# Optimization experiments

Measured on AMD Instinct MI355X. Metric: run time of the kernel, lower is better.

The kernel has to match this reference:

```python
import jax, jax.numpy as jnp
import numpy as np

N = 100000      # nodes
E = 640000      # total edges across all relations
D_IN = 128
D_OUT = 128
R = 8           # num_rel
B = 4           # num_bases


def setup_inputs() -> dict:
    key = jax.random.key(0)
    ks = jax.random.split(key, 7)
    return {
        "X": jax.random.normal(ks[0], (N, D_IN), dtype=jnp.float32),
        "edge_src": jax.random.randint(ks[1], (E,), 0, N, dtype=jnp.int32),
        "edge_dst": jax.random.randint(ks[2], (E,), 0, N, dtype=jnp.int32),
        "edge_rel": jax.random.randint(ks[3], (E,), 0, R, dtype=jnp.int32),
        "edge_val": jax.random.uniform(ks[4], (E,), dtype=jnp.float32),
        "w_bases": jax.random.normal(ks[5], (B, D_IN, D_OUT), dtype=jnp.float32) * 0.05,
        "w_rel": jax.random.normal(ks[6], (R, B), dtype=jnp.float32) * 0.5,
    }


def reference(X, edge_src, edge_dst, edge_rel, edge_val, w_bases, w_rel):
    # Per-relation SpMM: support_r = A_r @ X, where A_r rows are destinations.
    # Fuse all relations into one gather + one segmented scatter-add.
    msg = X[edge_src] * edge_val[:, None]                      # [E, D_IN]
    seg = edge_rel.astype(jnp.int32) * N + edge_dst            # combined (rel, dst) id
    supports = jax.ops.segment_sum(msg, seg, num_segments=R * N)
    supports = supports.reshape(R, N, D_IN)                    # == concat of per-rel supports
    # Basis-decomposed relation weights: w[r] = sum_b w_rel[r,b] * w_bases[b]
    w = jnp.einsum("rb,bio->rio", w_rel, w_bases)              # [R, D_IN, D_OUT]
    # cat(supports, dim=1) @ w.view(R*D_IN, D_OUT) == sum_r supports_r @ w_r
    out = jnp.einsum("rni,rio->no", supports, w)               # [N, D_OUT]
    return out
```

## Files before the change

### kernel.cpp

```cpp
#include <hip/hip_runtime.h>
#include <stdint.h>

#define D_IN 128
#define D_OUT 128
#define NREL 8
#define NBASE 4

typedef __attribute__((ext_vector_type(8))) short short8;
typedef __attribute__((ext_vector_type(4))) float floatx4;
typedef __attribute__((ext_vector_type(2))) float floatx2;

__device__ __forceinline__ unsigned short f2bf(float f) {
  unsigned int u = __float_as_uint(f);
  u += 0x7fffu + ((u >> 16) & 1u);
  return (unsigned short)(u >> 16);
}
__device__ __forceinline__ unsigned pack2bf(float lo, float hi) {
  return (unsigned)f2bf(lo) | ((unsigned)f2bf(hi) << 16);
}
__device__ __forceinline__ float bflo(unsigned int u) { return __uint_as_float(u << 16); }
__device__ __forceinline__ float bfhi(unsigned int u) { return __uint_as_float(u & 0xffff0000u); }

__global__ void k_prep(const float4* __restrict__ X, ushort4* __restrict__ Xb, int n4,
                       const float* __restrict__ w_bases, unsigned short* __restrict__ W2T,
                       const int* __restrict__ edst, int* __restrict__ counts, int E) {
  int i = blockIdx.x * blockDim.x + threadIdx.x;
  if (i < n4) {
    float4 v = X[i];
    ushort4 o;
    o.x = f2bf(v.x); o.y = f2bf(v.y); o.z = f2bf(v.z); o.w = f2bf(v.w);
    Xb[i] = o;
  }
  if (i < 128 * 512) {
    int o = i >> 9, c = i & 511;
    int k = c >> 2, b = c & 3;
    W2T[i] = f2bf(w_bases[(b * D_IN + k) * D_OUT + o]);
  }
  if (i < E) atomicAdd(&counts[edst[i]], 1);
}

__global__ void k_scan1(const int* __restrict__ counts, int* __restrict__ localsc,
                        int* __restrict__ bsum, int Nn) {
  __shared__ int s[256];
  int i = blockIdx.x * 256 + threadIdx.x;
  int v = (i < Nn) ? counts[i] : 0;
  s[threadIdx.x] = v;
  __syncthreads();
  for (int off = 1; off < 256; off <<= 1) {
    int t = 0;
    if (threadIdx.x >= off) t = s[threadIdx.x - off];
    __syncthreads();
    s[threadIdx.x] += t;
    __syncthreads();
  }
  if (i < Nn) localsc[i] = s[threadIdx.x] - v;
  if (threadIdx.x == 255) bsum[blockIdx.x] = s[255];
}

__global__ void k_scan23(const int* __restrict__ localsc, const int* __restrict__ bsum,
                         int* __restrict__ offsets, int* __restrict__ cursor, int Nn, int E) {
  __shared__ int red[256];
  int acc = 0;
  for (int j = threadIdx.x; j < blockIdx.x; j += 256) acc += bsum[j];
  red[threadIdx.x] = acc;
  __syncthreads();
  for (int off = 128; off > 0; off >>= 1) {
    if (threadIdx.x < off) red[threadIdx.x] += red[threadIdx.x + off];
    __syncthreads();
  }
  int pref = red[0];
  int i = blockIdx.x * 256 + threadIdx.x;
  if (i < Nn) {
    int v = localsc[i] + pref;
    offsets[i] = v;
    cursor[i] = v;
  }
  if (i == 0) offsets[Nn] = E;
}

__global__ void k_bucket(const int* __restrict__ src, const int* __restrict__ dst,
                         const int* __restrict__ rel, const float* __restrict__ val,
                         const float* __restrict__ w_rel, int* __restrict__ cursor,
                         unsigned* __restrict__ srcs, float4* __restrict__ coef, int E) {
  int i = blockIdx.x * blockDim.x + threadIdx.x;
  if (i < 64) srcs[E + i] = 0u;
  if (i >= E) return;
  int d = dst[i];
  int pos = atomicAdd(&cursor[d], 1);
  float v = val[i];
  const float4 w = *(const float4*)(w_rel + rel[i] * 4);
  srcs[pos] = (unsigned)src[i];
  coef[pos] = make_float4(v * w.x, v * w.y, v * w.z, v * w.w);
}

__global__ __launch_bounds__(256, 4)
void k_agg_gemm(const unsigned* __restrict__ esrcs, const float4* __restrict__ ecoef,
                const int* __restrict__ offsets, const unsigned* __restrict__ Xb2,
                const unsigned short* __restrict__ W2T, float* __restrict__ out, int Nn) {
  __shared__ __align__(16) unsigned short aggS[32][520];

  const int wave = threadIdx.x >> 6, lane = threadIdx.x & 63;
  const int d0 = blockIdx.x * 32 + wave * 8;
  const floatx2 zf2 = {0.f, 0.f};
  const uint64_t xbase = (uint64_t)Xb2;
  const unsigned loff = (unsigned)lane * 4u;

  int oidx = d0 + (lane < 8 ? lane : 8);
  if (oidx > Nn) oidx = Nn;
  const int offv = offsets[oidx];
  const int s0 = __builtin_amdgcn_readlane(offv, 0);
  const int e8 = __builtin_amdgcn_readlane(offv, 8);

  floatx2 a0 = zf2, a1 = zf2, a2 = zf2, a3 = zf2;
  int row = 0;
  int bnd = __builtin_amdgcn_readlane(offv, 1);

#define FLUSH()                                                      \
  do {                                                               \
    uint4 o_;                                                        \
    o_.x = pack2bf(a0.x, a1.x);                                      \
    o_.y = pack2bf(a2.x, a3.x);                                      \
    o_.z = pack2bf(a0.y, a1.y);                                      \
    o_.w = pack2bf(a2.y, a3.y);                                      \
    *(uint4*)&aggS[wave * 8 + row][lane * 8] = o_;                   \
    a0 = zf2; a1 = zf2; a2 = zf2; a3 = zf2;                          \
    ++row;                                                           \
    bnd = (row < 8) ? __builtin_amdgcn_readlane(offv, row + 1)       \
                    : 0x7fffffff;                                    \
  } while (0)

#define SSRC(S, BASE)                                                \
  do {                                                               \
    int b_ = (BASE);                                                 \
    s##S##0 = esrcs[b_];     s##S##1 = esrcs[b_ + 1];                \
    s##S##2 = esrcs[b_ + 2]; s##S##3 = esrcs[b_ + 3];                \
  } while (0)

#define GLOAD(Y, SRCID)                                              \
  do {                                                               \
    uint64_t ga_ = xbase + ((uint64_t)(SRCID) << 8);                 \
    asm volatile("global_load_dword %0, %1, %2"                      \
                 : "=v"(Y) : "v"(loff), "s"(ga_));                   \
  } while (0)

#define GATH(S)                                                      \
  do {                                                               \
    GLOAD(y##S##0, s##S##0); GLOAD(y##S##1, s##S##1);                \
    GLOAD(y##S##2, s##S##2); GLOAD(y##S##3, s##S##3);                \
  } while (0)

#define SCOEF(S, BASE)                                               \
  do {                                                               \
    int b_ = (BASE);                                                 \
    c##S##0 = ecoef[b_];     c##S##1 = ecoef[b_ + 1];                \
    c##S##2 = ecoef[b_ + 2]; c##S##3 = ecoef[b_ + 3];                \
  } while (0)

#define WAITG()                                                      \
  do {                                                               \
    asm volatile("s_waitcnt vmcnt(12)" ::: "memory");                \
    __builtin_amdgcn_sched_barrier(0);                               \
  } while (0)

#define ACCT1(EI, C, Y)                                              \
  do {                                                               \
    if ((EI) < e8) {                                                 \
      while ((EI) == bnd) FLUSH();                                   \
      floatx2 x_;                                                    \
      x_.x = bflo(Y);                                                \
      x_.y = bfhi(Y);                                                \
      a0 += (C).x * x_;                                              \
      a1 += (C).y * x_;                                              \
      a2 += (C).z * x_;                                              \
      a3 += (C).w * x_;                                              \
    }                                                                \
  } while (0)

#define ACCT4(S, EI0)                                                \
  do {                                                               \
    ACCT1((EI0), c##S##0, y##S##0);                                  \
    ACCT1((EI0) + 1, c##S##1, y##S##1);                              \
    ACCT1((EI0) + 2, c##S##2, y##S##2);                              \
    ACCT1((EI0) + 3, c##S##3, y##S##3);                              \
  } while (0)

  if (s0 < e8) {
    unsigned s00, s01, s02, s03, s10, s11, s12, s13, s20, s21, s22, s23;
    unsigned s30, s31, s32, s33, s40, s41, s42, s43, s50, s51, s52, s53;
    unsigned y00, y01, y02, y03, y10, y11, y12, y13, y20, y21, y22, y23;
    unsigned y30, y31, y32, y33, y40, y41, y42, y43, y50, y51, y52, y53;
    float4 c00, c01, c02, c03, c10, c11, c12, c13, c20, c21, c22, c23;
    float4 c30, c31, c32, c33, c40, c41, c42, c43, c50, c51, c52, c53;
    SSRC(0, s0); SSRC(1, s0 + 4); SSRC(2, s0 + 8); SSRC(3, s0 + 12);
    GATH(0); GATH(1); GATH(2);
    SCOEF(0, s0);
    int gi = s0;
    while (gi < e8) {
      GATH(3); SSRC(4, gi + 16); SCOEF(1, gi + 4);  WAITG(); ACCT4(0, gi);
      GATH(4); SSRC(5, gi + 20); SCOEF(2, gi + 8);  WAITG(); ACCT4(1, gi + 4);
      GATH(5); SSRC(0, gi + 24); SCOEF(3, gi + 12); WAITG(); ACCT4(2, gi + 8);
      GATH(0); SSRC(1, gi + 28); SCOEF(4, gi + 16); WAITG(); ACCT4(3, gi + 12);
      GATH(1); SSRC(2, gi + 32); SCOEF(5, gi + 20); WAITG(); ACCT4(4, gi + 16);
      GATH(2); SSRC(3, gi + 36); SCOEF(0, gi + 24); WAITG(); ACCT4(5, gi + 20);
      gi += 24;
    }
    __builtin_amdgcn_sched_barrier(0);
    asm volatile("s_waitcnt vmcnt(0) lgkmcnt(0)" ::: "memory");
    __builtin_amdgcn_sched_barrier(0);
  }
  while (row < 8) FLUSH();

  __syncthreads();

  const int q = lane >> 4, r16 = lane & 15;
  const int wn = wave * 32;
  const floatx4 zero = {0.f, 0.f, 0.f, 0.f};
  floatx4 acc[2][2];
  acc[0][0] = zero; acc[0][1] = zero; acc[1][0] = zero; acc[1][1] = zero;

#pragma unroll 4
  for (int k0 = 0; k0 < 512; k0 += 32) {
    int ka = k0 + q * 8;
    short8 af[2], bfv[2];
    af[0] = *(const short8*)&aggS[r16][ka];
    af[1] = *(const short8*)&aggS[16 + r16][ka];
    bfv[0] = *(const short8*)(W2T + (size_t)(wn + r16) * 512 + ka);
    bfv[1] = *(const short8*)(W2T + (size_t)(wn + 16 + r16) * 512 + ka);
#pragma unroll
    for (int i = 0; i < 2; ++i)
#pragma unroll
      for (int j = 0; j < 2; ++j)
        acc[i][j] = __builtin_amdgcn_mfma_f32_16x16x32_bf16(af[i], bfv[j], acc[i][j], 0, 0, 0);
  }

#pragma unroll
  for (int i = 0; i < 2; ++i) {
#pragma unroll
    for (int j = 0; j < 2; ++j) {
#pragma unroll
      for (int p = 0; p < 4; ++p) {
        int prow = i * 16 + q * 4 + p;
        int col = wn + j * 16 + r16;
        int grow = blockIdx.x * 32 + prow;
        if (grow < Nn) out[(size_t)grow * 128 + col] = acc[i][j][p];
      }
    }
  }
}

extern "C" void kernel_launch(void* const* d_in, const int* in_sizes, int n_in,
                              void* d_out, int out_size, void* d_ws, size_t ws_size,
                              hipStream_t stream) {
  const float* X = (const float*)d_in[0];
  const int* esrc = (const int*)d_in[1];
  const int* edst = (const int*)d_in[2];
  const int* erel = (const int*)d_in[3];
  const float* eval_ = (const float*)d_in[4];
  const float* w_bases = (const float*)d_in[5];
  const float* w_rel = (const float*)d_in[6];
  const int Nn = in_sizes[0] / D_IN;
  const int E = in_sizes[1];

  char* ws = (char*)d_ws;
  size_t off = 0;
  auto alloc = [&](size_t bytes) -> char* {
    char* p = ws + off;
    off += (bytes + 255) & ~(size_t)255;
    return p;
  };
  unsigned short* Xb = (unsigned short*)alloc((size_t)Nn * D_IN * 2);
  unsigned short* W2T = (unsigned short*)alloc((size_t)128 * 512 * 2);
  int* counts = (int*)alloc((size_t)Nn * 4);
  int* cursor = (int*)alloc((size_t)Nn * 4);
  int* offsets = (int*)alloc((size_t)(Nn + 1) * 4);
  int* localsc = (int*)alloc((size_t)Nn * 4);
  int* bsum = (int*)alloc(4096);
  unsigned* srcs = (unsigned*)alloc((size_t)(E + 64) * 4);
  float4* coef = (float4*)alloc((size_t)(E + 64) * 16);
  (void)ws_size;

  int n4 = Nn * D_IN / 4;
  hipMemsetAsync(counts, 0, (size_t)Nn * 4, stream);
  k_prep<<<(n4 + 255) / 256, 256, 0, stream>>>((const float4*)X, (ushort4*)Xb, n4,
                                               w_bases, W2T, edst, counts, E);

  int nb = (Nn + 255) / 256;
  k_scan1<<<nb, 256, 0, stream>>>(counts, localsc, bsum, Nn);
  k_scan23<<<nb, 256, 0, stream>>>(localsc, bsum, offsets, cursor, Nn, E);
  k_bucket<<<(E + 255) / 256, 256, 0, stream>>>(esrc, edst, erel, eval_, w_rel,
                                                cursor, srcs, coef, E);

  k_agg_gemm<<<(Nn + 31) / 32, 256, 0, stream>>>(srcs, coef, offsets,
                                                 (const unsigned*)Xb, W2T,
                                                 (float*)d_out, Nn);
}
```

Baseline: 267.7 us.

## Pack edge value and relation into one word, compute coefficients in aggregation

The bucketing kernel now stores a single 32-bit word per edge: the edge value with its low three mantissa bits replaced by the relation id. This replaces the 16-byte float4 of precomputed per-basis coefficients. The aggregation kernel keeps w_rel in shared memory and rebuilds the four coefficients per edge, cutting edge metadata traffic by roughly four times. Index loads are clamped to the segment end instead of relying on zero padding, and the prefetch schedule is reshuffled. The cost is a small precision loss in edge values and extra ALU and LDS reads per edge.

```diff
diff --git a/kernel.cpp b/kernel.cpp
--- a/kernel.cpp
+++ b/kernel.cpp
@@ -80,24 +80,25 @@
 
 __global__ void k_bucket(const int* __restrict__ src, const int* __restrict__ dst,
                          const int* __restrict__ rel, const float* __restrict__ val,
-                         const float* __restrict__ w_rel, int* __restrict__ cursor,
-                         unsigned* __restrict__ srcs, float4* __restrict__ coef, int E) {
+                         int* __restrict__ cursor, unsigned* __restrict__ srcs,
+                         unsigned* __restrict__ vrs, int E) {
   int i = blockIdx.x * blockDim.x + threadIdx.x;
-  if (i < 64) srcs[E + i] = 0u;
   if (i >= E) return;
   int d = dst[i];
   int pos = atomicAdd(&cursor[d], 1);
-  float v = val[i];
-  const float4 w = *(const float4*)(w_rel + rel[i] * 4);
   srcs[pos] = (unsigned)src[i];
-  coef[pos] = make_float4(v * w.x, v * w.y, v * w.z, v * w.w);
+  vrs[pos] = (__float_as_uint(val[i]) & ~7u) | (unsigned)rel[i];
 }
 
 __global__ __launch_bounds__(256, 4)
-void k_agg_gemm(const unsigned* __restrict__ esrcs, const float4* __restrict__ ecoef,
+void k_agg_gemm(const unsigned* __restrict__ esrcs, const unsigned* __restrict__ evrs,
                 const int* __restrict__ offsets, const unsigned* __restrict__ Xb2,
+                const float* __restrict__ w_rel_g,
                 const unsigned short* __restrict__ W2T, float* __restrict__ out, int Nn) {
   __shared__ __align__(16) unsigned short aggS[32][520];
+  __shared__ __align__(16) float wrS[NREL * NBASE];
+  if (threadIdx.x < NREL * NBASE) wrS[threadIdx.x] = w_rel_g[threadIdx.x];
+  __syncthreads();
 
   const int wave = threadIdx.x >> 6, lane = threadIdx.x & 63;
   const int d0 = blockIdx.x * 32 + wave * 8;
@@ -132,8 +133,23 @@
 #define SSRC(S, BASE)                                                \
   do {                                                               \
     int b_ = (BASE);                                                 \
-    s##S##0 = esrcs[b_];     s##S##1 = esrcs[b_ + 1];                \
-    s##S##2 = esrcs[b_ + 2]; s##S##3 = esrcs[b_ + 3];                \
+    int t0_ = b_ < ce ? b_ : ce;                                     \
+    int t1_ = b_ + 1 < ce ? b_ + 1 : ce;                             \
+    int t2_ = b_ + 2 < ce ? b_ + 2 : ce;                             \
+    int t3_ = b_ + 3 < ce ? b_ + 3 : ce;                             \
+    s##S##0 = esrcs[t0_]; s##S##1 = esrcs[t1_];                      \
+    s##S##2 = esrcs[t2_]; s##S##3 = esrcs[t3_];                      \
+  } while (0)
+
+#define SVR(S, BASE)                                                 \
+  do {                                                               \
+    int b_ = (BASE);                                                 \
+    int t0_ = b_ < ce ? b_ : ce;                                     \
+    int t1_ = b_ + 1 < ce ? b_ + 1 : ce;                             \
+    int t2_ = b_ + 2 < ce ? b_ + 2 : ce;                             \
+    int t3_ = b_ + 3 < ce ? b_ + 3 : ce;                             \
+    r##S##0 = evrs[t0_]; r##S##1 = evrs[t1_];                        \
+    r##S##2 = evrs[t2_]; r##S##3 = evrs[t3_];                        \
   } while (0)
 
 #define GLOAD(Y, SRCID)                                              \
@@ -149,11 +165,17 @@
     GLOAD(y##S##2, s##S##2); GLOAD(y##S##3, s##S##3);                \
   } while (0)
 
-#define SCOEF(S, BASE)                                               \
-  do {                                                               \
-    int b_ = (BASE);                                                 \
-    c##S##0 = ecoef[b_];     c##S##1 = ecoef[b_ + 1];                \
-    c##S##2 = ecoef[b_ + 2]; c##S##3 = ecoef[b_ + 3];                \
+#define COEF1(C, RV)                                                 \
+  do {                                                               \
+    const float4 w_ = *(const float4*)&wrS[((RV) & 7u) * 4];         \
+    const float v_ = __uint_as_float((RV) & ~7u);                    \
+    (C) = make_float4(v_ * w_.x, v_ * w_.y, v_ * w_.z, v_ * w_.w);   \
+  } while (0)
+
+#define COEF(S)                                                      \
+  do {                                                               \
+    COEF1(c##S##0, r##S##0); COEF1(c##S##1, r##S##1);                \
+    COEF1(c##S##2, r##S##2); COEF1(c##S##3, r##S##3);                \
   } while (0)
 
 #define WAITG()                                                      \
@@ -185,23 +207,28 @@
   } while (0)
 
   if (s0 < e8) {
+    const int ce = e8 - 1;
     unsigned s00, s01, s02, s03, s10, s11, s12, s13, s20, s21, s22, s23;
     unsigned s30, s31, s32, s33, s40, s41, s42, s43, s50, s51, s52, s53;
+    unsigned r00, r01, r02, r03, r10, r11, r12, r13, r20, r21, r22, r23;
+    unsigned r30, r31, r32, r33, r40, r41, r42, r43, r50, r51, r52, r53;
     unsigned y00, y01, y02, y03, y10, y11, y12, y13, y20, y21, y22, y23;
     unsigned y30, y31, y32, y33, y40, y41, y42, y43, y50, y51, y52, y53;
     float4 c00, c01, c02, c03, c10, c11, c12, c13, c20, c21, c22, c23;
     float4 c30, c31, c32, c33, c40, c41, c42, c43, c50, c51, c52, c53;
-    SSRC(0, s0); SSRC(1, s0 + 4); SSRC(2, s0 + 8); SSRC(3, s0 + 12);
+    SSRC(0, s0); SSRC(1, s0 + 4); SSRC(2, s0 + 8);
+    SSRC(3, s0 + 12); SSRC(4, s0 + 16);
+    SVR(0, s0); SVR(1, s0 + 4); SVR(2, s0 + 8); SVR(3, s0 + 12);
     GATH(0); GATH(1); GATH(2);
-    SCOEF(0, s0);
+    COEF(0); COEF(1);
     int gi = s0;
     while (gi < e8) {
-      GATH(3); SSRC(4, gi + 16); SCOEF(1, gi + 4);  WAITG(); ACCT4(0, gi);
-      GATH(4); SSRC(5, gi + 20); SCOEF(2, gi + 8);  WAITG(); ACCT4(1, gi + 4);
-      GATH(5); SSRC(0, gi + 24); SCOEF(3, gi + 12); WAITG(); ACCT4(2, gi + 8);
-      GATH(0); SSRC(1, gi + 28); SCOEF(4, gi + 16); WAITG(); ACCT4(3, gi + 12);
-      GATH(1); SSRC(2, gi + 32); SCOEF(5, gi + 20); WAITG(); ACCT4(4, gi + 16);
-      GATH(2); SSRC(3, gi + 36); SCOEF(0, gi + 24); WAITG(); ACCT4(5, gi + 20);
+      GATH(3); SSRC(5, gi + 20); SVR(4, gi + 16); COEF(2); WAITG(); ACCT4(0, gi);
+      GATH(4); SSRC(0, gi + 24); SVR(5, gi + 20); COEF(3); WAITG(); ACCT4(1, gi + 4);
+      GATH(5); SSRC(1, gi + 28); SVR(0, gi + 24); COEF(4); WAITG(); ACCT4(2, gi + 8);
+      GATH(0); SSRC(2, gi + 32); SVR(1, gi + 28); COEF(5); WAITG(); ACCT4(3, gi + 12);
+      GATH(1); SSRC(3, gi + 36); SVR(2, gi + 32); COEF(0); WAITG(); ACCT4(4, gi + 16);
+      GATH(2); SSRC(4, gi + 40); SVR(3, gi + 36); COEF(1); WAITG(); ACCT4(5, gi + 20);
       gi += 24;
     }
     __builtin_amdgcn_sched_barrier(0);
@@ -276,7 +303,7 @@
   int* localsc = (int*)alloc((size_t)Nn * 4);
   int* bsum = (int*)alloc(4096);
   unsigned* srcs = (unsigned*)alloc((size_t)(E + 64) * 4);
-  float4* coef = (float4*)alloc((size_t)(E + 64) * 16);
+  unsigned* vrs = (unsigned*)alloc((size_t)(E + 64) * 4);
   (void)ws_size;
 
   int n4 = Nn * D_IN / 4;
@@ -287,10 +314,10 @@
   int nb = (Nn + 255) / 256;
   k_scan1<<<nb, 256, 0, stream>>>(counts, localsc, bsum, Nn);
   k_scan23<<<nb, 256, 0, stream>>>(localsc, bsum, offsets, cursor, Nn, E);
-  k_bucket<<<(E + 255) / 256, 256, 0, stream>>>(esrc, edst, erel, eval_, w_rel,
-                                                cursor, srcs, coef, E);
-
-  k_agg_gemm<<<(Nn + 31) / 32, 256, 0, stream>>>(srcs, coef, offsets,
-                                                 (const unsigned*)Xb, W2T,
+  k_bucket<<<(E + 255) / 256, 256, 0, stream>>>(esrc, edst, erel, eval_,
+                                                cursor, srcs, vrs, E);
+
+  k_agg_gemm<<<(Nn + 31) / 32, 256, 0, stream>>>(srcs, vrs, offsets,
+                                                 (const unsigned*)Xb, w_rel, W2T,
                                                  (float*)d_out, Nn);
 }
```

Measured after the change: 249.9 us. -6.6%, faster.
